# Kernel tuning notes

Hardware: AMD Instinct MI355X
Metric: run time of the kernel (lower is better)

## Reference

```python
import jax, jax.numpy as jnp
import numpy as np

NUM_CLASSES = 256
EMBED_DIM = 1024
PATCH = 16
LN_EPS = 1e-5


def _sincos_pos_2d(hp, wp, dim):
    # Mirrors SemanticMapTokenizer._build_2d_sincos_pos_embed -> [hp, wp, dim]
    d_h = dim // 2
    d_w = dim - d_h
    d_h_even = (d_h // 2) * 2
    d_w_even = (d_w // 2) * 2

    def one_d(length, d_half):
        pos = jnp.arange(length, dtype=jnp.float32)
        omega = 1.0 / (10000.0 ** (jnp.arange(d_half, dtype=jnp.float32) / d_half))
        out = pos[:, None] * omega[None, :]  # [length, d_half]
        return jnp.concatenate([jnp.sin(out), jnp.cos(out)], axis=1)  # [length, 2*d_half]

    emb_h = one_d(hp, d_h_even // 2)  # [hp, d_h_even]
    emb_w = one_d(wp, d_w_even // 2)  # [wp, d_w_even]
    emb_h = jnp.broadcast_to(emb_h[:, None, :], (hp, wp, d_h_even))
    emb_w = jnp.broadcast_to(emb_w[None, :, :], (hp, wp, d_w_even))
    pos = jnp.concatenate([emb_h, emb_w], axis=-1)
    if pos.shape[-1] < dim:
        pos = jnp.concatenate([pos, jnp.zeros((hp, wp, dim - pos.shape[-1]), jnp.float32)], axis=-1)
    elif pos.shape[-1] > dim:
        pos = pos[:, :, :dim]
    return pos


def setup_inputs() -> dict:
    key = jax.random.key(0)
    k1, k2, k3 = jax.random.split(key, 3)
    semantic_map = jax.random.randint(k1, (2, 1, 512, 512), 0, NUM_CLASSES, dtype=jnp.int32)
    embed_table = jax.random.normal(k2, (NUM_CLASSES, EMBED_DIM), dtype=jnp.float32)
    gamma = jnp.ones((EMBED_DIM,), jnp.float32)
    beta = jnp.zeros((EMBED_DIM,), jnp.float32)
    return {"semantic_map": semantic_map, "embed_table": embed_table, "gamma": gamma, "beta": beta}


def reference(semantic_map, embed_table, gamma, beta):
    b, c, h, w = semantic_map.shape
    p = PATCH
    hp, wp = h // p, w // p
    d = embed_table.shape[1]
    # channel 0, round -> clamp -> int index
    idx = jnp.clip(jnp.round(semantic_map[:, 0].astype(jnp.float32)), 0, NUM_CLASSES - 1).astype(jnp.int32)
    pix = embed_table[idx]  # [B, H, W, D] -- large intermediate (gather)
    # AvgPool2d(kernel=stride=p): mean over non-overlapping p x p patches
    pooled = pix[:, : hp * p, : wp * p, :].reshape(b, hp, p, wp, p, d).mean(axis=(2, 4))  # [B, hp, wp, D]
    pooled = pooled + _sincos_pos_2d(hp, wp, d)[None]
    tokens = pooled.reshape(b, hp * wp, d)
    # LayerNorm over last dim
    mu = tokens.mean(axis=-1, keepdims=True)
    var = jnp.mean(jnp.square(tokens - mu), axis=-1, keepdims=True)
    tokens = (tokens - mu) * jax.lax.rsqrt(var + LN_EPS) * gamma + beta
    return tokens
```

## Files before the change

### kernel.cpp

```cpp
#include <hip/hip_runtime.h>

#define IMG   512
#define NCLS  256
#define DIM   1024
#define HPW   32
#define MAGIC 0x5EEDC0DEu

typedef short bf16x8 __attribute__((ext_vector_type(8)));
typedef float f32x4  __attribute__((ext_vector_type(4)));

__device__ inline ushort bf16rne(float v) {
    unsigned u = __float_as_uint(v);
    return (ushort)((u + 0x7fffu + ((u >> 16) & 1u)) >> 16);
}

__global__ __launch_bounds__(256)
void prep(const int* __restrict__ smap, const float* __restrict__ table,
          ushort* __restrict__ Tt2, ushort* __restrict__ Ab)
{
    __shared__ ushort   tile[16][264];
    __shared__ unsigned cnt[32 * NCLS];
    const int t   = threadIdx.x;
    const int bid = blockIdx.x;

    if (bid < 64) {
        const int dtile = bid;
        const float* src = table + (size_t)t * DIM + dtile * 16;
        #pragma unroll
        for (int q = 0; q < 4; ++q) {
            const float4 v = *reinterpret_cast<const float4*>(src + q * 4);
            tile[q * 4 + 0][t] = bf16rne(v.x);
            tile[q * 4 + 1][t] = bf16rne(v.y);
            tile[q * 4 + 2][t] = bf16rne(v.z);
            tile[q * 4 + 3][t] = bf16rne(v.w);
        }
        __syncthreads();
        const int ks   = t >> 5;
        const int g    = (t >> 3) & 3;
        const int c0   = (t & 7) * 2;
        const int cls0 = ks * 32 + g * 8;
        uint4* dst = reinterpret_cast<uint4*>(Tt2 + (size_t)dtile * 4096 + (size_t)t * 16);
        dst[0] = *reinterpret_cast<const uint4*>(&tile[c0][cls0]);
        dst[1] = *reinterpret_cast<const uint4*>(&tile[c0 + 1][cls0]);
    } else {
        const int grp  = bid - 64;
        const int tok0 = grp * 32;
        const int b    = tok0 >> 10;
        const int ph   = (tok0 >> 5) & 31;

        #pragma unroll
        for (int i = t; i < 32 * NCLS; i += 256) cnt[i] = 0u;
        __syncthreads();

        const int row  = t >> 4;
        const int col0 = (t & 15) * 32;
        const int* bp = smap + ((size_t)b * IMG + (size_t)(ph * 16 + row)) * IMG + col0;
        #pragma unroll
        for (int q4 = 0; q4 < 8; ++q4) {
            const int4 q = *reinterpret_cast<const int4*>(bp + q4 * 4);
            unsigned* hp = &cnt[((col0 + q4 * 4) >> 4) * NCLS];
            atomicAdd(&hp[min(max(q.x, 0), NCLS - 1)], 1u);
            atomicAdd(&hp[min(max(q.y, 0), NCLS - 1)], 1u);
            atomicAdd(&hp[min(max(q.z, 0), NCLS - 1)], 1u);
            atomicAdd(&hp[min(max(q.w, 0), NCLS - 1)], 1u);
        }
        __syncthreads();

        ushort* ab = Ab + (size_t)grp * 8192;
        #pragma unroll
        for (int i = t; i < 8192; i += 256)
            ab[i] = (ushort)(__float_as_uint((float)cnt[i] * (1.f / 256.f)) >> 16);
    }
}

__global__ __launch_bounds__(1024)
void gemm_ln(const ushort* __restrict__ Ab, const ushort* __restrict__ Tt2,
             const float* __restrict__ gamma, const float* __restrict__ beta,
             float* __restrict__ out, float* __restrict__ pstats,
             unsigned* __restrict__ flags)
{
    __shared__ ushort cntb[32][264];
    __shared__ float  red[16][2][4][4][2];
    __shared__ float  sstage[4][32][2];
    __shared__ float  mu_s[32], rs_s[32];

    const int t    = threadIdx.x;
    const int lane = t & 63;
    const int w    = t >> 6;
    const int c    = lane & 15;
    const int g    = lane >> 4;

    const int grp  = blockIdx.x >> 2;
    const int dq   = blockIdx.x & 3;
    const int tok0 = grp * 32;
    const int ph   = (tok0 >> 5) & 31;

    {
        const uint4 v = reinterpret_cast<const uint4*>(Ab + (size_t)grp * 8192)[t];
        const int idx = t * 8;
        *reinterpret_cast<uint4*>(&cntb[idx >> 8][idx & 255]) = v;
    }
    __syncthreads();

    f32x4 acc0 = (f32x4){0.f, 0.f, 0.f, 0.f};
    f32x4 acc1 = (f32x4){0.f, 0.f, 0.f, 0.f};
    const ushort* bt = Tt2 + (size_t)(dq * 16 + w) * 4096 + (size_t)lane * 8;
    #pragma unroll 2
    for (int ks = 0; ks < 8; ++ks) {
        const bf16x8 bf = *reinterpret_cast<const bf16x8*>(bt + ks * 512);
        const bf16x8 a0 = *reinterpret_cast<const bf16x8*>(&cntb[c][ks * 32 + g * 8]);
        const bf16x8 a1 = *reinterpret_cast<const bf16x8*>(&cntb[16 + c][ks * 32 + g * 8]);
        acc0 = __builtin_amdgcn_mfma_f32_16x16x32_bf16(a0, bf, acc0, 0, 0, 0);
        acc1 = __builtin_amdgcn_mfma_f32_16x16x32_bf16(a1, bf, acc1, 0, 0, 0);
    }

    {
        const float omega = exp2f((float)(w * 16 + c) * (-13.287712379549449f / 256.f));
        if (dq < 2) {
            float sv, cv; __sincosf((float)ph * omega, &sv, &cv);
            const float v = (dq & 1) ? cv : sv;
            #pragma unroll
            for (int i = 0; i < 4; ++i) { acc0[i] += v; acc1[i] += v; }
        } else {
            #pragma unroll
            for (int i = 0; i < 4; ++i) {
                float sv, cv;
                __sincosf((float)(g * 4 + i) * omega, &sv, &cv);
                acc0[i] += (dq & 1) ? cv : sv;
                __sincosf((float)(16 + g * 4 + i) * omega, &sv, &cv);
                acc1[i] += (dq & 1) ? cv : sv;
            }
        }
    }

    float ls0[4], ls20[4], ls1[4], ls21[4];
    #pragma unroll
    for (int i = 0; i < 4; ++i) {
        ls0[i] = acc0[i]; ls20[i] = acc0[i] * acc0[i];
        ls1[i] = acc1[i]; ls21[i] = acc1[i] * acc1[i];
    }
    #pragma unroll
    for (int off = 1; off < 16; off <<= 1) {
        #pragma unroll
        for (int i = 0; i < 4; ++i) {
            ls0[i]  += __shfl_xor(ls0[i],  off, 64);
            ls20[i] += __shfl_xor(ls20[i], off, 64);
            ls1[i]  += __shfl_xor(ls1[i],  off, 64);
            ls21[i] += __shfl_xor(ls21[i], off, 64);
        }
    }
    if (c == 0) {
        #pragma unroll
        for (int i = 0; i < 4; ++i) {
            red[w][0][g][i][0] = ls0[i]; red[w][0][g][i][1] = ls20[i];
            red[w][1][g][i][0] = ls1[i]; red[w][1][g][i][1] = ls21[i];
        }
    }
    __syncthreads();

    if (t < 64) {
        const int token = t >> 1, which = t & 1;
        const int mf = token >> 4, gg = (token >> 2) & 3, ii = token & 3;
        float S = 0.f;
        #pragma unroll
        for (int ww = 0; ww < 16; ++ww) S += red[ww][mf][gg][ii][which];
        __hip_atomic_store(&pstats[((size_t)blockIdx.x * 32 + token) * 2 + which], S,
                           __ATOMIC_RELAXED, __HIP_MEMORY_SCOPE_SYSTEM);
    }
    __syncthreads();
    if (t == 0)
        __hip_atomic_store(&flags[blockIdx.x], MAGIC,
                           __ATOMIC_RELEASE, __HIP_MEMORY_SCOPE_SYSTEM);

    if (t < 4) {
        while (__hip_atomic_load(&flags[grp * 4 + t], __ATOMIC_ACQUIRE,
                                 __HIP_MEMORY_SCOPE_SYSTEM) != MAGIC) {}
    }
    __syncthreads();
    if (t < 256) {
        const int dq2 = t >> 6, token = (t & 63) >> 1, which = t & 1;
        sstage[dq2][token][which] =
            pstats[((size_t)(grp * 4 + dq2) * 32 + token) * 2 + which];
    }
    __syncthreads();
    if (t < 32) {
        float S = 0.f, S2 = 0.f;
        #pragma unroll
        for (int q = 0; q < 4; ++q) { S += sstage[q][t][0]; S2 += sstage[q][t][1]; }
        const float mu = S * (1.f / DIM);
        mu_s[t] = mu;
        rs_s[t] = rsqrtf(S2 * (1.f / DIM) - mu * mu + 1e-5f);
    }
    __syncthreads();

    {
        const int d = dq * 256 + w * 16 + c;
        const float gv = gamma[d], bv = beta[d];
        #pragma unroll
        for (int i = 0; i < 4; ++i) {
            const int r0 = g * 4 + i;
            out[(size_t)(tok0 + r0) * DIM + d]      = (acc0[i] - mu_s[r0])      * rs_s[r0]      * gv + bv;
            out[(size_t)(tok0 + 16 + r0) * DIM + d] = (acc1[i] - mu_s[16 + r0]) * rs_s[16 + r0] * gv + bv;
        }
    }
}

extern "C" void kernel_launch(void* const* d_in, const int* in_sizes, int n_in,
                              void* d_out, int out_size, void* d_ws, size_t ws_size,
                              hipStream_t stream) {
    const int*   smap  = (const int*)d_in[0];
    const float* table = (const float*)d_in[1];
    const float* gamma = (const float*)d_in[2];
    const float* beta  = (const float*)d_in[3];
    float*       out   = (float*)d_out;

    const int batches = in_sizes[0] / (IMG * IMG);
    const int tokens  = batches * HPW * HPW;
    const int ngrp    = tokens / 32;

    ushort*   Tt2    = (ushort*)d_ws;
    ushort*   Ab     = Tt2 + (size_t)64 * 4096;
    float*    pstats = (float*)(Ab + (size_t)ngrp * 8192);
    unsigned* flags  = (unsigned*)(pstats + (size_t)ngrp * 4 * 32 * 2);

    prep<<<64 + ngrp, 256, 0, stream>>>(smap, table, Tt2, Ab);
    gemm_ln<<<ngrp * 4, 1024, 0, stream>>>(Ab, Tt2, gamma, beta, out, pstats, flags);
}
```

Before: 22.89 us.

## Replace inter-block flag spin barrier with separate LayerNorm kernel

```diff
diff --git a/kernel.cpp b/kernel.cpp
--- a/kernel.cpp
+++ b/kernel.cpp
@@ -4,7 +4,6 @@
 #define NCLS  256
 #define DIM   1024
 #define HPW   32
-#define MAGIC 0x5EEDC0DEu
 
 typedef short bf16x8 __attribute__((ext_vector_type(8)));
 typedef float f32x4  __attribute__((ext_vector_type(4)));
@@ -74,15 +73,11 @@
 }
 
 __global__ __launch_bounds__(1024)
-void gemm_ln(const ushort* __restrict__ Ab, const ushort* __restrict__ Tt2,
-             const float* __restrict__ gamma, const float* __restrict__ beta,
-             float* __restrict__ out, float* __restrict__ pstats,
-             unsigned* __restrict__ flags)
+void gemm_part(const ushort* __restrict__ Ab, const ushort* __restrict__ Tt2,
+               float* __restrict__ preLN, float* __restrict__ pstats)
 {
     __shared__ ushort cntb[32][264];
     __shared__ float  red[16][2][4][4][2];
-    __shared__ float  sstage[4][32][2];
-    __shared__ float  mu_s[32], rs_s[32];
 
     const int t    = threadIdx.x;
     const int lane = t & 63;
@@ -90,8 +85,9 @@
     const int c    = lane & 15;
     const int g    = lane >> 4;
 
-    const int grp  = blockIdx.x >> 2;
-    const int dq   = blockIdx.x & 3;
+    const int bid  = blockIdx.x;
+    const int grp  = bid >> 2;
+    const int dq   = bid & 3;
     const int tok0 = grp * 32;
     const int ph   = (tok0 >> 5) & 31;
 
@@ -105,13 +101,16 @@
     f32x4 acc0 = (f32x4){0.f, 0.f, 0.f, 0.f};
     f32x4 acc1 = (f32x4){0.f, 0.f, 0.f, 0.f};
     const ushort* bt = Tt2 + (size_t)(dq * 16 + w) * 4096 + (size_t)lane * 8;
-    #pragma unroll 2
+    bf16x8 bfv[8];
+    #pragma unroll
+    for (int ks = 0; ks < 8; ++ks)
+        bfv[ks] = *reinterpret_cast<const bf16x8*>(bt + ks * 512);
+    #pragma unroll
     for (int ks = 0; ks < 8; ++ks) {
-        const bf16x8 bf = *reinterpret_cast<const bf16x8*>(bt + ks * 512);
         const bf16x8 a0 = *reinterpret_cast<const bf16x8*>(&cntb[c][ks * 32 + g * 8]);
         const bf16x8 a1 = *reinterpret_cast<const bf16x8*>(&cntb[16 + c][ks * 32 + g * 8]);
-        acc0 = __builtin_amdgcn_mfma_f32_16x16x32_bf16(a0, bf, acc0, 0, 0, 0);
-        acc1 = __builtin_amdgcn_mfma_f32_16x16x32_bf16(a1, bf, acc1, 0, 0, 0);
+        acc0 = __builtin_amdgcn_mfma_f32_16x16x32_bf16(a0, bfv[ks], acc0, 0, 0, 0);
+        acc1 = __builtin_amdgcn_mfma_f32_16x16x32_bf16(a1, bfv[ks], acc1, 0, 0, 0);
     }
 
     {
@@ -164,44 +163,63 @@
         float S = 0.f;
         #pragma unroll
         for (int ww = 0; ww < 16; ++ww) S += red[ww][mf][gg][ii][which];
-        __hip_atomic_store(&pstats[((size_t)blockIdx.x * 32 + token) * 2 + which], S,
-                           __ATOMIC_RELAXED, __HIP_MEMORY_SCOPE_SYSTEM);
-    }
-    __syncthreads();
-    if (t == 0)
-        __hip_atomic_store(&flags[blockIdx.x], MAGIC,
-                           __ATOMIC_RELEASE, __HIP_MEMORY_SCOPE_SYSTEM);
-
-    if (t < 4) {
-        while (__hip_atomic_load(&flags[grp * 4 + t], __ATOMIC_ACQUIRE,
-                                 __HIP_MEMORY_SCOPE_SYSTEM) != MAGIC) {}
-    }
-    __syncthreads();
-    if (t < 256) {
-        const int dq2 = t >> 6, token = (t & 63) >> 1, which = t & 1;
-        sstage[dq2][token][which] =
-            pstats[((size_t)(grp * 4 + dq2) * 32 + token) * 2 + which];
-    }
-    __syncthreads();
-    if (t < 32) {
+        pstats[(size_t)bid * 64 + token * 2 + which] = S;
+    }
+    {
+        const int ds = w * 16 + c;
+        #pragma unroll
+        for (int i = 0; i < 4; ++i) {
+            const int r0 = g * 4 + i;
+            preLN[((size_t)bid * 32 + r0) * 256 + ds]        = acc0[i];
+            preLN[((size_t)bid * 32 + 16 + r0) * 256 + ds]   = acc1[i];
+        }
+    }
+}
+
+__global__ __launch_bounds__(1024)
+void ln_final(const float* __restrict__ preLN, const float* __restrict__ pstats,
+              const float* __restrict__ gamma, const float* __restrict__ beta,
+              float* __restrict__ out)
+{
+    __shared__ float mu_s[8], rs_s[8];
+    const int t    = threadIdx.x;
+    const int tok0 = blockIdx.x * 8;
+    const int grp  = tok0 >> 5;
+    const int rb   = tok0 & 31;
+
+    if (t < 8) {
         float S = 0.f, S2 = 0.f;
         #pragma unroll
-        for (int q = 0; q < 4; ++q) { S += sstage[q][t][0]; S2 += sstage[q][t][1]; }
+        for (int dq = 0; dq < 4; ++dq) {
+            const size_t base = ((size_t)(grp * 4 + dq) * 32 + rb + t) * 2;
+            S  += pstats[base + 0];
+            S2 += pstats[base + 1];
+        }
         const float mu = S * (1.f / DIM);
         mu_s[t] = mu;
         rs_s[t] = rsqrtf(S2 * (1.f / DIM) - mu * mu + 1e-5f);
     }
     __syncthreads();
 
-    {
-        const int d = dq * 256 + w * 16 + c;
-        const float gv = gamma[d], bv = beta[d];
-        #pragma unroll
-        for (int i = 0; i < 4; ++i) {
-            const int r0 = g * 4 + i;
-            out[(size_t)(tok0 + r0) * DIM + d]      = (acc0[i] - mu_s[r0])      * rs_s[r0]      * gv + bv;
-            out[(size_t)(tok0 + 16 + r0) * DIM + d] = (acc1[i] - mu_s[16 + r0]) * rs_s[16 + r0] * gv + bv;
-        }
+    #pragma unroll
+    for (int it = 0; it < 2; ++it) {
+        const int idx = it * 1024 + t;
+        const int tk  = idx >> 8;
+        const int f4  = idx & 255;
+        const int d0  = f4 * 4;
+        const int dq  = d0 >> 8;
+        const int ds  = d0 & 255;
+        const float4 v  = *reinterpret_cast<const float4*>(
+            preLN + ((size_t)(grp * 4 + dq) * 32 + rb + tk) * 256 + ds);
+        const float4 gv = *reinterpret_cast<const float4*>(gamma + d0);
+        const float4 bv = *reinterpret_cast<const float4*>(beta + d0);
+        const float mu = mu_s[tk], rs = rs_s[tk];
+        float4 o;
+        o.x = (v.x - mu) * rs * gv.x + bv.x;
+        o.y = (v.y - mu) * rs * gv.y + bv.y;
+        o.z = (v.z - mu) * rs * gv.z + bv.z;
+        o.w = (v.w - mu) * rs * gv.w + bv.w;
+        *reinterpret_cast<float4*>(out + (size_t)(tok0 + tk) * DIM + d0) = o;
     }
 }
 
@@ -218,11 +236,12 @@
     const int tokens  = batches * HPW * HPW;
     const int ngrp    = tokens / 32;
 
-    ushort*   Tt2    = (ushort*)d_ws;
-    ushort*   Ab     = Tt2 + (size_t)64 * 4096;
-    float*    pstats = (float*)(Ab + (size_t)ngrp * 8192);
-    unsigned* flags  = (unsigned*)(pstats + (size_t)ngrp * 4 * 32 * 2);
+    ushort* Tt2    = (ushort*)d_ws;
+    ushort* Ab     = Tt2 + (size_t)64 * 4096;
+    float*  preLN  = (float*)(Ab + (size_t)ngrp * 8192);
+    float*  pstats = preLN + (size_t)tokens * DIM;
 
     prep<<<64 + ngrp, 256, 0, stream>>>(smap, table, Tt2, Ab);
-    gemm_ln<<<ngrp * 4, 1024, 0, stream>>>(Ab, Tt2, gamma, beta, out, pstats, flags);
-}
+    gemm_part<<<ngrp * 4, 1024, 0, stream>>>(Ab, Tt2, preLN, pstats);
+    ln_final<<<tokens / 8, 1024, 0, stream>>>(preLN, pstats, gamma, beta, out);
+}
```

Result: no change. 23.25 us (+1.6%).

## Fuse prep and GEMM+LayerNorm into one kernel with flag-based table handoff

Applied to the files above, without the earlier changes.

```diff
diff --git a/kernel.cpp b/kernel.cpp
--- a/kernel.cpp
+++ b/kernel.cpp
@@ -4,6 +4,7 @@
 #define NCLS  256
 #define DIM   1024
 #define HPW   32
+#define NT    1024
 #define MAGIC 0x5EEDC0DEu
 
 typedef short bf16x8 __attribute__((ext_vector_type(8)));
@@ -14,75 +15,19 @@
     return (ushort)((u + 0x7fffu + ((u >> 16) & 1u)) >> 16);
 }
 
-__global__ __launch_bounds__(256)
-void prep(const int* __restrict__ smap, const float* __restrict__ table,
-          ushort* __restrict__ Tt2, ushort* __restrict__ Ab)
+__global__ __launch_bounds__(NT)
+void fused_one(const int* __restrict__ smap, const float* __restrict__ table,
+               const float* __restrict__ gamma, const float* __restrict__ beta,
+               float* __restrict__ out, ushort* __restrict__ Tt2,
+               float* __restrict__ pstats, unsigned* __restrict__ flags,
+               unsigned* __restrict__ flags2)
 {
-    __shared__ ushort   tile[16][264];
     __shared__ unsigned cnt[32 * NCLS];
-    const int t   = threadIdx.x;
-    const int bid = blockIdx.x;
-
-    if (bid < 64) {
-        const int dtile = bid;
-        const float* src = table + (size_t)t * DIM + dtile * 16;
-        #pragma unroll
-        for (int q = 0; q < 4; ++q) {
-            const float4 v = *reinterpret_cast<const float4*>(src + q * 4);
-            tile[q * 4 + 0][t] = bf16rne(v.x);
-            tile[q * 4 + 1][t] = bf16rne(v.y);
-            tile[q * 4 + 2][t] = bf16rne(v.z);
-            tile[q * 4 + 3][t] = bf16rne(v.w);
-        }
-        __syncthreads();
-        const int ks   = t >> 5;
-        const int g    = (t >> 3) & 3;
-        const int c0   = (t & 7) * 2;
-        const int cls0 = ks * 32 + g * 8;
-        uint4* dst = reinterpret_cast<uint4*>(Tt2 + (size_t)dtile * 4096 + (size_t)t * 16);
-        dst[0] = *reinterpret_cast<const uint4*>(&tile[c0][cls0]);
-        dst[1] = *reinterpret_cast<const uint4*>(&tile[c0 + 1][cls0]);
-    } else {
-        const int grp  = bid - 64;
-        const int tok0 = grp * 32;
-        const int b    = tok0 >> 10;
-        const int ph   = (tok0 >> 5) & 31;
-
-        #pragma unroll
-        for (int i = t; i < 32 * NCLS; i += 256) cnt[i] = 0u;
-        __syncthreads();
-
-        const int row  = t >> 4;
-        const int col0 = (t & 15) * 32;
-        const int* bp = smap + ((size_t)b * IMG + (size_t)(ph * 16 + row)) * IMG + col0;
-        #pragma unroll
-        for (int q4 = 0; q4 < 8; ++q4) {
-            const int4 q = *reinterpret_cast<const int4*>(bp + q4 * 4);
-            unsigned* hp = &cnt[((col0 + q4 * 4) >> 4) * NCLS];
-            atomicAdd(&hp[min(max(q.x, 0), NCLS - 1)], 1u);
-            atomicAdd(&hp[min(max(q.y, 0), NCLS - 1)], 1u);
-            atomicAdd(&hp[min(max(q.z, 0), NCLS - 1)], 1u);
-            atomicAdd(&hp[min(max(q.w, 0), NCLS - 1)], 1u);
-        }
-        __syncthreads();
-
-        ushort* ab = Ab + (size_t)grp * 8192;
-        #pragma unroll
-        for (int i = t; i < 8192; i += 256)
-            ab[i] = (ushort)(__float_as_uint((float)cnt[i] * (1.f / 256.f)) >> 16);
-    }
-}
-
-__global__ __launch_bounds__(1024)
-void gemm_ln(const ushort* __restrict__ Ab, const ushort* __restrict__ Tt2,
-             const float* __restrict__ gamma, const float* __restrict__ beta,
-             float* __restrict__ out, float* __restrict__ pstats,
-             unsigned* __restrict__ flags)
-{
-    __shared__ ushort cntb[32][264];
-    __shared__ float  red[16][2][4][4][2];
-    __shared__ float  sstage[4][32][2];
-    __shared__ float  mu_s[32], rs_s[32];
+    __shared__ ushort   pk[1024];
+    __shared__ ushort   cntb[32][264];
+    __shared__ float    red[16][2][4][4][2];
+    __shared__ float    sstage[4][32][2];
+    __shared__ float    mu_s[32], rs_s[32];
 
     const int t    = threadIdx.x;
     const int lane = t & 63;
@@ -90,28 +35,88 @@
     const int c    = lane & 15;
     const int g    = lane >> 4;
 
-    const int grp  = blockIdx.x >> 2;
-    const int dq   = blockIdx.x & 3;
+    const int bid  = blockIdx.x;
+    const int grp  = bid >> 2;
+    const int dq   = bid & 3;
     const int tok0 = grp * 32;
-    const int ph   = (tok0 >> 5) & 31;
+    const int b    = grp >> 5;
+    const int ph   = grp & 31;
+
+    const int dtile = bid >> 2;
+    const int q     = bid & 3;
+
+    if (t < 256) {
+        const int cls  = q * 64 + (t >> 2);
+        const int quad = t & 3;
+        const float4 v = *reinterpret_cast<const float4*>(
+            table + (size_t)cls * DIM + dtile * 16 + quad * 4);
+        const int ks = cls >> 5, gg = (cls >> 3) & 3, j = cls & 7;
+        ushort* dst = pk + (ks & 1) * 512 + gg * 128 + j;
+        dst[(quad * 4 + 0) * 8] = bf16rne(v.x);
+        dst[(quad * 4 + 1) * 8] = bf16rne(v.y);
+        dst[(quad * 4 + 2) * 8] = bf16rne(v.z);
+        dst[(quad * 4 + 3) * 8] = bf16rne(v.w);
+    } else {
+        for (int i = t - 256; i < 32 * NCLS; i += 768) cnt[i] = 0u;
+    }
+    __syncthreads();
+
+    if (t < 512) {
+        const unsigned val = (unsigned)pk[t * 2] | ((unsigned)pk[t * 2 + 1] << 16);
+        __hip_atomic_store((unsigned*)Tt2 + (size_t)dtile * 2048 + q * 512 + t, val,
+                           __ATOMIC_RELAXED, __HIP_MEMORY_SCOPE_SYSTEM);
+    }
+    __syncthreads();
+
+    if (t == 0)
+        __hip_atomic_store(&flags[bid], MAGIC, __ATOMIC_RELEASE, __HIP_MEMORY_SCOPE_SYSTEM);
 
     {
-        const uint4 v = reinterpret_cast<const uint4*>(Ab + (size_t)grp * 8192)[t];
-        const int idx = t * 8;
-        *reinterpret_cast<uint4*>(&cntb[idx >> 8][idx & 255]) = v;
+        const int row  = t >> 6;
+        const int col0 = (t & 63) * 8;
+        const int* bp = smap + ((size_t)b * IMG + (size_t)(ph * 16 + row)) * IMG + col0;
+        const int4 q0 = *reinterpret_cast<const int4*>(bp);
+        const int4 q1 = *reinterpret_cast<const int4*>(bp + 4);
+        unsigned* hp = &cnt[(col0 >> 4) * NCLS];
+        atomicAdd(&hp[min(max(q0.x, 0), NCLS - 1)], 1u);
+        atomicAdd(&hp[min(max(q0.y, 0), NCLS - 1)], 1u);
+        atomicAdd(&hp[min(max(q0.z, 0), NCLS - 1)], 1u);
+        atomicAdd(&hp[min(max(q0.w, 0), NCLS - 1)], 1u);
+        atomicAdd(&hp[min(max(q1.x, 0), NCLS - 1)], 1u);
+        atomicAdd(&hp[min(max(q1.y, 0), NCLS - 1)], 1u);
+        atomicAdd(&hp[min(max(q1.z, 0), NCLS - 1)], 1u);
+        atomicAdd(&hp[min(max(q1.w, 0), NCLS - 1)], 1u);
+    }
+    __syncthreads();
+
+    for (int i = t; i < 32 * NCLS; i += NT)
+        cntb[i >> 8][i & 255] = (ushort)(__float_as_uint((float)cnt[i] * (1.f / 256.f)) >> 16);
+
+    if (t < 64) {
+        while (__hip_atomic_load(&flags[dq * 64 + t], __ATOMIC_RELAXED,
+                                 __HIP_MEMORY_SCOPE_SYSTEM) != MAGIC) {}
+    }
+    __syncthreads();
+    if (t == 0) {
+        unsigned x = __hip_atomic_load(&flags[dq * 64], __ATOMIC_ACQUIRE,
+                                       __HIP_MEMORY_SCOPE_SYSTEM);
+        asm volatile("" :: "v"(x));
     }
     __syncthreads();
 
     f32x4 acc0 = (f32x4){0.f, 0.f, 0.f, 0.f};
     f32x4 acc1 = (f32x4){0.f, 0.f, 0.f, 0.f};
     const ushort* bt = Tt2 + (size_t)(dq * 16 + w) * 4096 + (size_t)lane * 8;
-    #pragma unroll 2
+    bf16x8 bfv[8];
+    #pragma unroll
+    for (int ks = 0; ks < 8; ++ks)
+        bfv[ks] = *reinterpret_cast<const bf16x8*>(bt + ks * 512);
+    #pragma unroll
     for (int ks = 0; ks < 8; ++ks) {
-        const bf16x8 bf = *reinterpret_cast<const bf16x8*>(bt + ks * 512);
         const bf16x8 a0 = *reinterpret_cast<const bf16x8*>(&cntb[c][ks * 32 + g * 8]);
         const bf16x8 a1 = *reinterpret_cast<const bf16x8*>(&cntb[16 + c][ks * 32 + g * 8]);
-        acc0 = __builtin_amdgcn_mfma_f32_16x16x32_bf16(a0, bf, acc0, 0, 0, 0);
-        acc1 = __builtin_amdgcn_mfma_f32_16x16x32_bf16(a1, bf, acc1, 0, 0, 0);
+        acc0 = __builtin_amdgcn_mfma_f32_16x16x32_bf16(a0, bfv[ks], acc0, 0, 0, 0);
+        acc1 = __builtin_amdgcn_mfma_f32_16x16x32_bf16(a1, bfv[ks], acc1, 0, 0, 0);
     }
 
     {
@@ -164,29 +169,35 @@
         float S = 0.f;
         #pragma unroll
         for (int ww = 0; ww < 16; ++ww) S += red[ww][mf][gg][ii][which];
-        __hip_atomic_store(&pstats[((size_t)blockIdx.x * 32 + token) * 2 + which], S,
+        __hip_atomic_store(&pstats[(size_t)bid * 64 + token * 2 + which], S,
                            __ATOMIC_RELAXED, __HIP_MEMORY_SCOPE_SYSTEM);
     }
     __syncthreads();
     if (t == 0)
-        __hip_atomic_store(&flags[blockIdx.x], MAGIC,
-                           __ATOMIC_RELEASE, __HIP_MEMORY_SCOPE_SYSTEM);
+        __hip_atomic_store(&flags2[bid], MAGIC, __ATOMIC_RELEASE, __HIP_MEMORY_SCOPE_SYSTEM);
 
     if (t < 4) {
-        while (__hip_atomic_load(&flags[grp * 4 + t], __ATOMIC_ACQUIRE,
+        while (__hip_atomic_load(&flags2[grp * 4 + t], __ATOMIC_RELAXED,
                                  __HIP_MEMORY_SCOPE_SYSTEM) != MAGIC) {}
     }
     __syncthreads();
+    if (t == 0) {
+        unsigned x = __hip_atomic_load(&flags2[grp * 4], __ATOMIC_ACQUIRE,
+                                       __HIP_MEMORY_SCOPE_SYSTEM);
+        asm volatile("" :: "v"(x));
+    }
+    __syncthreads();
+
     if (t < 256) {
         const int dq2 = t >> 6, token = (t & 63) >> 1, which = t & 1;
         sstage[dq2][token][which] =
-            pstats[((size_t)(grp * 4 + dq2) * 32 + token) * 2 + which];
+            pstats[(size_t)(grp * 4 + dq2) * 64 + token * 2 + which];
     }
     __syncthreads();
     if (t < 32) {
         float S = 0.f, S2 = 0.f;
         #pragma unroll
-        for (int q = 0; q < 4; ++q) { S += sstage[q][t][0]; S2 += sstage[q][t][1]; }
+        for (int qq = 0; qq < 4; ++qq) { S += sstage[qq][t][0]; S2 += sstage[qq][t][1]; }
         const float mu = S * (1.f / DIM);
         mu_s[t] = mu;
         rs_s[t] = rsqrtf(S2 * (1.f / DIM) - mu * mu + 1e-5f);
@@ -216,13 +227,13 @@
 
     const int batches = in_sizes[0] / (IMG * IMG);
     const int tokens  = batches * HPW * HPW;
-    const int ngrp    = tokens / 32;
+    const int nblk    = (tokens / 32) * 4;
 
     ushort*   Tt2    = (ushort*)d_ws;
-    ushort*   Ab     = Tt2 + (size_t)64 * 4096;
-    float*    pstats = (float*)(Ab + (size_t)ngrp * 8192);
-    unsigned* flags  = (unsigned*)(pstats + (size_t)ngrp * 4 * 32 * 2);
-
-    prep<<<64 + ngrp, 256, 0, stream>>>(smap, table, Tt2, Ab);
-    gemm_ln<<<ngrp * 4, 1024, 0, stream>>>(Ab, Tt2, gamma, beta, out, pstats, flags);
+    float*    pstats = (float*)(Tt2 + (size_t)64 * 4096);
+    unsigned* flags  = (unsigned*)(pstats + (size_t)256 * 64);
+    unsigned* flags2 = flags + 256;
+
+    fused_one<<<nblk, NT, 0, stream>>>(smap, table, gamma, beta, out,
+                                       Tt2, pstats, flags, flags2);
 }
```

Result: slower. 23.49 us (+2.6%).
